# Performance work log

Hardware: AMD Instinct MI355X
Metric: run time of the kernel (lower is better)

The kernel has to match this reference:

```python
import jax, jax.numpy as jnp
import numpy as np

B, N, D_VIS, D_LBL = 64, 256, 2048, 512
H, F_OUT = 8, 256            # n_heads, gat_out_per_head_dim
D_IN = D_VIS + D_LBL         # 2560, GAT input dim
D_GAT = H * F_OUT            # 2048, concat-heads output dim
D_EMB = 512                  # final_embedding_dim
ALPHA = 0.2                  # LeakyReLU negative slope


def setup_inputs() -> dict:
    key = jax.random.key(0)
    ks = jax.random.split(key, 9)
    visual_features = jax.random.normal(ks[0], (B, D_VIS), jnp.float32)
    labels_features = jax.random.normal(ks[1], (N, D_LBL), jnp.float32)
    adj = (jax.random.uniform(ks[2], (N, N)) < 0.1).astype(jnp.float32)
    label_adj_matrix = jnp.maximum(adj, jnp.eye(N, dtype=jnp.float32))
    s = 1.0 / np.sqrt(D_IN)
    W_gat = jax.random.uniform(ks[3], (D_IN, H, F_OUT), jnp.float32, -s, s)
    a_src = jax.random.uniform(ks[4], (H, F_OUT), jnp.float32, -s, s)
    a_dst = jax.random.uniform(ks[5], (H, F_OUT), jnp.float32, -s, s)
    sg = 1.0 / np.sqrt(D_GAT)
    pool_q = jax.random.uniform(ks[6], (D_GAT,), jnp.float32, -sg, sg)
    fc_W = jax.random.uniform(ks[7], (D_GAT, D_EMB), jnp.float32, -sg, sg)
    fc_b = jax.random.uniform(ks[8], (D_EMB,), jnp.float32, -sg, sg)
    return {"visual_features": visual_features, "labels_features": labels_features,
            "label_adj_matrix": label_adj_matrix, "W_gat": W_gat, "a_src": a_src,
            "a_dst": a_dst, "pool_q": pool_q, "fc_W": fc_W, "fc_b": fc_b}


def reference(visual_features, labels_features, label_adj_matrix,
              W_gat, a_src, a_dst, pool_q, fc_W, fc_b):
    # Build per-sample contextualized label node features: (B, N, D_IN)
    x = jnp.concatenate(
        [jnp.broadcast_to(labels_features[None], (B, N, D_LBL)),
         jnp.broadcast_to(visual_features[:, None, :], (B, N, D_VIS))], axis=-1)
    # Multi-head GAT layer, batched over B (the torch code loops over B)
    Wh = jnp.einsum('bnd,dhf->bnhf', x, W_gat)            # (B, N, H, F)
    src = jnp.einsum('bnhf,hf->bhn', Wh, a_src)           # (B, H, N)
    dst = jnp.einsum('bnhf,hf->bhn', Wh, a_dst)           # (B, H, N)
    e = src[:, :, :, None] + dst[:, :, None, :]           # (B, H, N, N)
    e = jnp.where(e > 0, e, ALPHA * e)                    # LeakyReLU
    mask = (label_adj_matrix > 0)[None, None]             # (1, 1, N, N)
    scores = jnp.where(mask, e, jnp.float32(-9e15))
    attn = jax.nn.softmax(scores, axis=-1)                # (B, H, N, N)
    out = jnp.einsum('bhij,bjhf->bihf', attn, Wh)         # (B, N, H, F)
    out = jax.nn.elu(out.reshape(B, N, D_GAT))            # concat heads + ELU
    # attention pooling over label nodes
    pw = jax.nn.softmax(jnp.einsum('bnd,d->bn', out, pool_q), axis=-1)
    pooled = jnp.einsum('bn,bnd->bd', pw, out)            # (B, D_GAT)
    return pooled @ fc_W + fc_b                           # (B, D_EMB)
```

## Files before the change

### kernel.cpp

```cpp
#include <hip/hip_runtime.h>
#include <hip/hip_bf16.h>
#include <math.h>

#define BB 64
#define NN 256
#define D_VIS 2048
#define D_LBL 512
#define HH 8
#define FF 256
#define DG 2048
#define DE 512
#define ALPHA 0.2f
#define PSTRIDE 264
#define NSPLIT 4

using bf16 = __hip_bfloat16;
using short8 = __attribute__((ext_vector_type(8))) short;
using f32x4  = __attribute__((ext_vector_type(4))) float;
__device__ __forceinline__ float b2f(bf16 x) { return __bfloat162float(x); }
__device__ __forceinline__ unsigned short f2bs(float x) {
    bf16 h = __float2bfloat16(x);
    unsigned short u;
    __builtin_memcpy(&u, &h, 2);
    return u;
}
__device__ __forceinline__ float bs2f(unsigned short u) {
    unsigned int x = (unsigned int)u << 16;
    float f;
    __builtin_memcpy(&f, &x, 4);
    return f;
}

__global__ void __launch_bounds__(256) k_wh(const float* __restrict__ labels,
                                            const float* __restrict__ visual,
                                            const float* __restrict__ Wg,
                                            unsigned short* __restrict__ WhLbT,
                                            float* __restrict__ WhVz,
                                            const float* __restrict__ aSrc,
                                            const float* __restrict__ aDst,
                                            float* __restrict__ srcLp,
                                            float* __restrict__ dstLp,
                                            float* __restrict__ srcVp,
                                            float* __restrict__ dstVp,
                                            const float* __restrict__ adj,
                                            unsigned short* __restrict__ abits) {
    const int t = threadIdx.x;
    const int y = blockIdx.y;
    if (y == 8) {
        if (t < 128) {
            const int r = t >> 4, s = t & 15;
            const int i = blockIdx.x * 8 + r;
            unsigned int bits = 0;
#pragma unroll
            for (int jj = 0; jj < 8; ++jj) {
                const float2 av = *(const float2*)(adj + (size_t)i * NN + 2 * s + 32 * jj);
                bits |= (av.x > 0.f ? 1u : 0u) << (2 * jj);
                bits |= (av.y > 0.f ? 1u : 0u) << (2 * jj + 1);
            }
            abits[i * 16 + s] = (unsigned short)bits;
        }
        return;
    }

    __shared__ unsigned short As[2][64][72];
    __shared__ unsigned short Bs[2][64][72];
    const int w = t >> 6;
    const int lane = t & 63;
    const int l15 = lane & 15, quad = lane >> 4;
    const int n0 = blockIdx.x * 64;
    const int p2 = blockIdx.x & 3;
    const bool isL = (y < 4);
    const int m0  = isL ? y * 64 : 0;
    const int z   = isL ? 0 : (y - 4);
    const int kb0 = z * 512;
    const float* A = isL ? labels : visual;
    const int lda  = isL ? D_LBL : D_VIS;
    const float* Wb = Wg + (isL ? 0 : (size_t)D_LBL * DG);

    f32x4 acc[4];
#pragma unroll
    for (int mi = 0; mi < 4; ++mi) acc[mi] = (f32x4){0.f, 0.f, 0.f, 0.f};

    float4 ra[4], rb[4];
    auto load_tile = [&](int kc) {
        const int kb = kb0 + kc * 64;
#pragma unroll
        for (int p = 0; p < 4; ++p) {
            const int idx = t + 256 * p;
            const int r = idx >> 4, q4 = idx & 15;
            ra[p] = *(const float4*)(A + (size_t)(m0 + r) * lda + kb + 4 * q4);
        }
#pragma unroll
        for (int p = 0; p < 4; ++p) {
            const int kk = (t >> 4) + 16 * p;
            const int c4 = (t & 15) * 4;
            rb[p] = *(const float4*)(Wb + (size_t)(kb + kk) * DG + n0 + c4);
        }
    };
    auto store_tile = [&](int buf) {
#pragma unroll
        for (int p = 0; p < 4; ++p) {
            const int idx = t + 256 * p;
            const int r = idx >> 4, q4 = idx & 15;
            unsigned short s4[4] = {f2bs(ra[p].x), f2bs(ra[p].y), f2bs(ra[p].z), f2bs(ra[p].w)};
            __builtin_memcpy(&As[buf][r][4 * q4], s4, 8);
        }
#pragma unroll
        for (int p = 0; p < 4; ++p) {
            const int kk = (t >> 4) + 16 * p;
            const int c4 = (t & 15) * 4;
            Bs[buf][c4 + 0][kk] = f2bs(rb[p].x);
            Bs[buf][c4 + 1][kk] = f2bs(rb[p].y);
            Bs[buf][c4 + 2][kk] = f2bs(rb[p].z);
            Bs[buf][c4 + 3][kk] = f2bs(rb[p].w);
        }
    };

    load_tile(0);
    store_tile(0);
    __syncthreads();
    for (int kc = 0; kc < 8; ++kc) {
        const int cur = kc & 1;
        if (kc < 7) load_tile(kc + 1);
#pragma unroll
        for (int ks = 0; ks < 2; ++ks) {
            const short8 bf = *(const short8*)&Bs[cur][w * 16 + l15][ks * 32 + quad * 8];
#pragma unroll
            for (int mi = 0; mi < 4; ++mi) {
                const short8 af = *(const short8*)&As[cur][mi * 16 + l15][ks * 32 + quad * 8];
                acc[mi] = __builtin_amdgcn_mfma_f32_16x16x32_bf16(af, bf, acc[mi], 0, 0, 0);
            }
        }
        if (kc < 7) store_tile(cur ^ 1);
        __syncthreads();
    }
    const int col = n0 + w * 16 + l15;
    const int h = col >> 8;
    const float as = aSrc[col], ad = aDst[col];
    if (isL) {
#pragma unroll
        for (int mi = 0; mi < 4; ++mi) {
            unsigned short s4[4];
#pragma unroll
            for (int r = 0; r < 4; ++r) s4[r] = f2bs(acc[mi][r]);
            __builtin_memcpy(&WhLbT[(size_t)col * NN + m0 + mi * 16 + quad * 4], s4, 8);
        }
#pragma unroll
        for (int mi = 0; mi < 4; ++mi)
#pragma unroll
            for (int r = 0; r < 4; ++r) {
                float sv = acc[mi][r] * as;
                float dv = acc[mi][r] * ad;
#pragma unroll
                for (int off = 1; off < 16; off <<= 1) {
                    sv += __shfl_xor(sv, off);
                    dv += __shfl_xor(dv, off);
                }
                if (l15 == 0) {
                    const int row = m0 + mi * 16 + quad * 4 + r;
                    srcLp[(p2 * NN + row) * HH + h] = sv;
                    dstLp[(p2 * NN + row) * HH + h] = dv;
                }
            }
    } else {
        float* Wv = WhVz + (size_t)z * BB * DG;
#pragma unroll
        for (int mi = 0; mi < 4; ++mi)
#pragma unroll
            for (int r = 0; r < 4; ++r)
                Wv[(size_t)(mi * 16 + quad * 4 + r) * DG + col] = acc[mi][r];
        const int pv = p2 * 4 + z;
#pragma unroll
        for (int mi = 0; mi < 4; ++mi)
#pragma unroll
            for (int r = 0; r < 4; ++r) {
                float sv = acc[mi][r] * as;
                float dv = acc[mi][r] * ad;
#pragma unroll
                for (int off = 1; off < 16; off <<= 1) {
                    sv += __shfl_xor(sv, off);
                    dv += __shfl_xor(dv, off);
                }
                if (l15 == 0) {
                    const int row = mi * 16 + quad * 4 + r;
                    srcVp[(pv * BB + row) * HH + h] = sv;
                    dstVp[(pv * BB + row) * HH + h] = dv;
                }
            }
    }
}

__global__ void __launch_bounds__(512, 4) k_gat(const unsigned short* __restrict__ WhLbT,
                                                const float* __restrict__ WhVz,
                                                const float* __restrict__ srcLp,
                                                const float* __restrict__ dstLp,
                                                const float* __restrict__ srcVp,
                                                const float* __restrict__ dstVp,
                                                const unsigned short* __restrict__ abits,
                                                const float* __restrict__ pool_q,
                                                bf16* __restrict__ outb,
                                                float* __restrict__ ps_p) {
    const int bid = blockIdx.x;
    const int h = bid & 7;
    const int b = bid >> 3;
    const int t = threadIdx.x;
    const int w = t >> 6;
    const int lane = t & 63;
    const int l15 = lane & 15, quad = lane >> 4;

    __shared__ __align__(16) unsigned short Pl[64][PSTRIDE];
    __shared__ __align__(16) float dls2[2 * NN];
    __shared__ float slsA[NN], slsC[NN];
    __shared__ float inv[64];
    __shared__ float psl[8][64];

    if (t < NN) {
        float dl = 0.f, sl = 0.f;
#pragma unroll
        for (int p = 0; p < 4; ++p) {
            dl += dstLp[(p * NN + t) * HH + h];
            sl += srcLp[(p * NN + t) * HH + h];
        }
        dls2[2 * t]     = __expf(dl);
        dls2[2 * t + 1] = __expf(ALPHA * dl);
        float c = 0.f;
#pragma unroll
        for (int p = 0; p < 16; ++p)
            c += srcVp[(p * BB + b) * HH + h] + dstVp[(p * BB + b) * HH + h];
        const float u = c + sl;
        slsA[t] = __expf(u);
        slsC[t] = __expf(ALPHA * u);
    }
    const int n0 = w * 32;
    float wv[2] = {0.f, 0.f};
#pragma unroll
    for (int z = 0; z < 4; ++z)
#pragma unroll
        for (int ni = 0; ni < 2; ++ni)
            wv[ni] += WhVz[(size_t)z * BB * DG + (size_t)b * DG + h * FF + n0 + ni * 16 + l15];
    const float pqv0 = pool_q[h * FF + n0 + l15];
    const float pqv1 = pool_q[h * FF + n0 + 16 + l15];
    const unsigned short* wb = WhLbT + (size_t)(h * FF + n0 + l15) * NN + quad * 8;
    __syncthreads();

    for (int it = 0; it < 4; ++it) {
        const int i0 = it * 64;

        {
            const int g = lane >> 4, s = lane & 15;
#pragma unroll
            for (int rr = 0; rr < 2; ++rr) {
                const int iloc = w * 8 + rr * 4 + g;
                const int i = i0 + iloc;
                const unsigned int mb = abits[i * 16 + s];
                const float Ai = slsA[i], Ci = slsC[i];
                float pr[16];
                float sum = 0.f;
#pragma unroll
                for (int jj = 0; jj < 8; ++jj) {
                    const int j0 = 2 * s + 32 * jj;
                    const float4 bd = *(const float4*)&dls2[2 * j0];
                    float p0 = fmaxf(Ai * bd.x, Ci * bd.y);
                    float p1 = fmaxf(Ai * bd.z, Ci * bd.w);
                    p0 = (mb & (1u << (2 * jj)))     ? p0 : 0.f;
                    p1 = (mb & (1u << (2 * jj + 1))) ? p1 : 0.f;
                    pr[2 * jj] = p0; pr[2 * jj + 1] = p1;
                    sum += p0 + p1;
                }
#pragma unroll
                for (int off = 1; off < 16; off <<= 1) sum += __shfl_xor(sum, off);
                if (s == 0) inv[iloc] = 1.0f / sum;
#pragma unroll
                for (int jj = 0; jj < 8; ++jj) {
                    const unsigned int pk =
                        ((unsigned int)f2bs(pr[2 * jj + 1]) << 16) | f2bs(pr[2 * jj]);
                    *(unsigned int*)&Pl[iloc][2 * s + 32 * jj] = pk;
                }
            }
        }
        __syncthreads();

        f32x4 acc[4][2];
#pragma unroll
        for (int mi = 0; mi < 4; ++mi)
#pragma unroll
            for (int ni = 0; ni < 2; ++ni) acc[mi][ni] = (f32x4){0.f, 0.f, 0.f, 0.f};

        short8 bc0 = *(const short8*)(wb);
        short8 bc1 = *(const short8*)(wb + (size_t)16 * NN);
#pragma unroll
        for (int kc = 0; kc < 8; ++kc) {
            short8 bn0, bn1;
            if (kc < 7) {
                bn0 = *(const short8*)(wb + (kc + 1) * 32);
                bn1 = *(const short8*)(wb + (size_t)16 * NN + (kc + 1) * 32);
            }
            short8 a[4];
#pragma unroll
            for (int mi = 0; mi < 4; ++mi)
                a[mi] = *(const short8*)&Pl[mi * 16 + l15][kc * 32 + quad * 8];
#pragma unroll
            for (int mi = 0; mi < 4; ++mi)
                acc[mi][0] = __builtin_amdgcn_mfma_f32_16x16x32_bf16(a[mi], bc0, acc[mi][0], 0, 0, 0);
#pragma unroll
            for (int mi = 0; mi < 4; ++mi)
                acc[mi][1] = __builtin_amdgcn_mfma_f32_16x16x32_bf16(a[mi], bc1, acc[mi][1], 0, 0, 0);
            bc0 = bn0; bc1 = bn1;
        }

#pragma unroll
        for (int mi = 0; mi < 4; ++mi)
#pragma unroll
            for (int r = 0; r < 4; ++r) {
                const int row = mi * 16 + quad * 4 + r;
                const float ivr = inv[row];
                bf16* orow = outb + ((size_t)(b * NN + i0 + row)) * DG + h * FF + n0;
                float x0 = fmaf(acc[mi][0][r], ivr, wv[0]);
                float x1 = fmaf(acc[mi][1][r], ivr, wv[1]);
                x0 = x0 > 0.f ? x0 : (__expf(x0) - 1.0f);
                x1 = x1 > 0.f ? x1 : (__expf(x1) - 1.0f);
                orow[l15]      = __float2bfloat16(x0);
                orow[16 + l15] = __float2bfloat16(x1);
                float dot = fmaf(x0, pqv0, x1 * pqv1);
#pragma unroll
                for (int off = 1; off < 16; off <<= 1) dot += __shfl_xor(dot, off);
                if (l15 == 0) psl[w][row] = dot;
            }
        __syncthreads();
        if (t < 64) {
            float s = 0.f;
#pragma unroll
            for (int ww = 0; ww < 8; ++ww) s += psl[ww][t];
            ps_p[((size_t)h * BB + b) * NN + i0 + t] = s;
        }
    }
}

__global__ void __launch_bounds__(256) k_pool(const bf16* __restrict__ outb,
                                              const float* __restrict__ ps_p,
                                              float* __restrict__ pooled_p,
                                              const float* __restrict__ fcb,
                                              float* __restrict__ out) {
    const int dt = blockIdx.x;
    const int b  = blockIdx.y;
    const int ns = blockIdx.z;
    const int t  = threadIdx.x;
    if (dt == 0 && ns == 0) {
        out[b * DE + t]       = fcb[t];
        out[b * DE + 256 + t] = fcb[256 + t];
    }
    __shared__ float wsm[NN];
    __shared__ float redm[4];
    __shared__ float reds[4];
    float v = 0.f;
#pragma unroll
    for (int s = 0; s < 8; ++s)
        v += ps_p[((size_t)s * BB + b) * NN + t];
    float m = v;
#pragma unroll
    for (int off = 32; off; off >>= 1) m = fmaxf(m, __shfl_xor(m, off));
    if ((t & 63) == 0) redm[t >> 6] = m;
    __syncthreads();
    m = fmaxf(fmaxf(redm[0], redm[1]), fmaxf(redm[2], redm[3]));
    const float e = __expf(v - m);
    float s = e;
#pragma unroll
    for (int off = 32; off; off >>= 1) s += __shfl_xor(s, off);
    if ((t & 63) == 0) reds[t >> 6] = s;
    __syncthreads();
    s = reds[0] + reds[1] + reds[2] + reds[3];
    wsm[t] = e / s;
    __syncthreads();
    const int d0 = dt * 512 + t * 2;
    const int nb = ns * 64;
    float a0 = 0.f, a1 = 0.f;
    const bf16* base = outb + (size_t)b * NN * DG + d0;
#pragma unroll 8
    for (int n = 0; n < 64; ++n) {
        unsigned int q = *(const unsigned int*)(base + (size_t)(nb + n) * DG);
        const float wn = wsm[nb + n];
        a0 = fmaf(wn, bs2f((unsigned short)(q & 0xffff)), a0);
        a1 = fmaf(wn, bs2f((unsigned short)(q >> 16)), a1);
    }
    float2 r2 = {a0, a1};
    *(float2*)(pooled_p + ((size_t)(ns * BB + b)) * DG + d0) = r2;
}

__global__ void __launch_bounds__(256) k_mgemm(const float* __restrict__ Ap,
                                               const float* __restrict__ W, int ldw,
                                               float* __restrict__ C, int ldc,
                                               int kSlice, int kIters) {
    __shared__ unsigned short As[32][72];
    __shared__ unsigned short Bs[64][72];
    const int t = threadIdx.x;
    const int w = t >> 6;
    const int lane = t & 63;
    const int l15 = lane & 15, quad = lane >> 4;
    const int n0 = blockIdx.x * 64;
    const int m0 = blockIdx.y * 32;
    const int kb0 = blockIdx.z * kSlice;
    f32x4 acc[2];
    acc[0] = (f32x4){0.f, 0.f, 0.f, 0.f};
    acc[1] = (f32x4){0.f, 0.f, 0.f, 0.f};
    for (int kc = 0; kc < kIters; ++kc) {
        const int kb = kb0 + kc * 64;
#pragma unroll
        for (int p = 0; p < 2; ++p) {
            const int idx = t + 256 * p;
            const int r = idx >> 4, q4 = idx & 15;
            const float* ap = Ap + (size_t)(m0 + r) * DG + kb + 4 * q4;
            const float4 v0 = *(const float4*)(ap);
            const float4 v1 = *(const float4*)(ap + (size_t)BB * DG);
            const float4 v2 = *(const float4*)(ap + (size_t)2 * BB * DG);
            const float4 v3 = *(const float4*)(ap + (size_t)3 * BB * DG);
            const float vx = v0.x + v1.x + v2.x + v3.x;
            const float vy = v0.y + v1.y + v2.y + v3.y;
            const float vz = v0.z + v1.z + v2.z + v3.z;
            const float vw = v0.w + v1.w + v2.w + v3.w;
            unsigned short s4[4] = {f2bs(vx), f2bs(vy), f2bs(vz), f2bs(vw)};
            __builtin_memcpy(&As[r][4 * q4], s4, 8);
        }
#pragma unroll
        for (int p = 0; p < 4; ++p) {
            const int kk = (t >> 4) + 16 * p;
            const int c4 = (t & 15) * 4;
            const float4 v = *(const float4*)(W + (size_t)(kb + kk) * ldw + n0 + c4);
            Bs[c4 + 0][kk] = f2bs(v.x);
            Bs[c4 + 1][kk] = f2bs(v.y);
            Bs[c4 + 2][kk] = f2bs(v.z);
            Bs[c4 + 3][kk] = f2bs(v.w);
        }
        __syncthreads();
#pragma unroll
        for (int ks = 0; ks < 2; ++ks) {
            const short8 bf = *(const short8*)&Bs[w * 16 + l15][ks * 32 + quad * 8];
#pragma unroll
            for (int mi = 0; mi < 2; ++mi) {
                const short8 af = *(const short8*)&As[mi * 16 + l15][ks * 32 + quad * 8];
                acc[mi] = __builtin_amdgcn_mfma_f32_16x16x32_bf16(af, bf, acc[mi], 0, 0, 0);
            }
        }
        __syncthreads();
    }
    const int col = n0 + w * 16 + l15;
#pragma unroll
    for (int mi = 0; mi < 2; ++mi)
#pragma unroll
        for (int r = 0; r < 4; ++r)
            atomicAdd(&C[(size_t)(m0 + mi * 16 + quad * 4 + r) * ldc + col], acc[mi][r]);
}

extern "C" void kernel_launch(void* const* d_in, const int* in_sizes, int n_in,
                              void* d_out, int out_size, void* d_ws, size_t ws_size,
                              hipStream_t stream) {
    (void)in_sizes; (void)n_in; (void)out_size; (void)ws_size;
    const float* visual = (const float*)d_in[0];
    const float* labels = (const float*)d_in[1];
    const float* adj    = (const float*)d_in[2];
    const float* Wg     = (const float*)d_in[3];
    const float* a_src  = (const float*)d_in[4];
    const float* a_dst  = (const float*)d_in[5];
    const float* pool_q = (const float*)d_in[6];
    const float* fcW    = (const float*)d_in[7];
    const float* fcb    = (const float*)d_in[8];
    float* out = (float*)d_out;

    float* ws_f     = (float*)d_ws;
    float* WhVz     = ws_f;
    float* srcLp    = WhVz + 4 * BB * DG;
    float* dstLp    = srcLp + 4 * NN * HH;
    float* srcVp    = dstLp + 4 * NN * HH;
    float* dstVp    = srcVp + 16 * BB * HH;
    float* ps_p     = dstVp + 16 * BB * HH;
    float* pooled_p = ps_p + 8 * BB * NN;
    bf16*  outb     = (bf16*)(pooled_p + NSPLIT * BB * DG);
    unsigned short* WhLbT = (unsigned short*)(outb + (size_t)BB * NN * DG);
    unsigned short* abits = WhLbT + (size_t)DG * NN;

    k_wh<<<dim3(DG / 64, 9), 256, 0, stream>>>(labels, visual, Wg, WhLbT, WhVz,
                                               a_src, a_dst, srcLp, dstLp, srcVp, dstVp,
                                               adj, abits);

    k_gat<<<BB * HH, 512, 0, stream>>>(WhLbT, WhVz, srcLp, dstLp, srcVp, dstVp,
                                       abits, pool_q, outb, ps_p);

    k_pool<<<dim3(4, BB, NSPLIT), 256, 0, stream>>>(outb, ps_p, pooled_p, fcb, out);

    k_mgemm<<<dim3(DE / 64, BB / 32, 16), 256, 0, stream>>>(
        pooled_p, fcW, DE, out, DE, 128, 2);
}
```

Baseline: 164.0 us.

## Deepen k_wh load prefetch and widen k_pool vector loads with finer node split

```diff
diff --git a/kernel.cpp b/kernel.cpp
--- a/kernel.cpp
+++ b/kernel.cpp
@@ -12,7 +12,7 @@
 #define DE 512
 #define ALPHA 0.2f
 #define PSTRIDE 264
-#define NSPLIT 4
+#define NSPLIT 16
 
 using bf16 = __hip_bfloat16;
 using short8 = __attribute__((ext_vector_type(8))) short;
@@ -81,8 +81,8 @@
 #pragma unroll
     for (int mi = 0; mi < 4; ++mi) acc[mi] = (f32x4){0.f, 0.f, 0.f, 0.f};
 
-    float4 ra[4], rb[4];
-    auto load_tile = [&](int kc) {
+    float4 raA[4], rbA[4], raB[4], rbB[4];
+    auto load_tile = [&](int kc, float4 (&ra)[4], float4 (&rb)[4]) {
         const int kb = kb0 + kc * 64;
 #pragma unroll
         for (int p = 0; p < 4; ++p) {
@@ -97,7 +97,7 @@
             rb[p] = *(const float4*)(Wb + (size_t)(kb + kk) * DG + n0 + c4);
         }
     };
-    auto store_tile = [&](int buf) {
+    auto store_tile = [&](int buf, float4 (&ra)[4], float4 (&rb)[4]) {
 #pragma unroll
         for (int p = 0; p < 4; ++p) {
             const int idx = t + 256 * p;
@@ -115,23 +115,32 @@
             Bs[buf][c4 + 3][kk] = f2bs(rb[p].w);
         }
     };
-
-    load_tile(0);
-    store_tile(0);
+    auto mfma_step = [&](int buf) {
+#pragma unroll
+        for (int ks = 0; ks < 2; ++ks) {
+            const short8 bf = *(const short8*)&Bs[buf][w * 16 + l15][ks * 32 + quad * 8];
+#pragma unroll
+            for (int mi = 0; mi < 4; ++mi) {
+                const short8 af = *(const short8*)&As[buf][mi * 16 + l15][ks * 32 + quad * 8];
+                acc[mi] = __builtin_amdgcn_mfma_f32_16x16x32_bf16(af, bf, acc[mi], 0, 0, 0);
+            }
+        }
+    };
+
+    load_tile(0, raA, rbA);
+    load_tile(1, raB, rbB);
+    store_tile(0, raA, rbA);
     __syncthreads();
-    for (int kc = 0; kc < 8; ++kc) {
-        const int cur = kc & 1;
-        if (kc < 7) load_tile(kc + 1);
-#pragma unroll
-        for (int ks = 0; ks < 2; ++ks) {
-            const short8 bf = *(const short8*)&Bs[cur][w * 16 + l15][ks * 32 + quad * 8];
-#pragma unroll
-            for (int mi = 0; mi < 4; ++mi) {
-                const short8 af = *(const short8*)&As[cur][mi * 16 + l15][ks * 32 + quad * 8];
-                acc[mi] = __builtin_amdgcn_mfma_f32_16x16x32_bf16(af, bf, acc[mi], 0, 0, 0);
-            }
-        }
-        if (kc < 7) store_tile(cur ^ 1);
+#pragma unroll
+    for (int kp = 0; kp < 4; ++kp) {
+        const int kc = kp * 2;
+        if (kc + 2 < 8) load_tile(kc + 2, raA, rbA);
+        mfma_step(0);
+        store_tile(1, raB, rbB);
+        __syncthreads();
+        if (kc + 3 < 8) load_tile(kc + 3, raB, rbB);
+        mfma_step(1);
+        if (kc + 2 < 8) store_tile(0, raA, rbA);
         __syncthreads();
     }
     const int col = n0 + w * 16 + l15;
@@ -341,11 +350,10 @@
                                               float* __restrict__ pooled_p,
                                               const float* __restrict__ fcb,
                                               float* __restrict__ out) {
-    const int dt = blockIdx.x;
-    const int b  = blockIdx.y;
-    const int ns = blockIdx.z;
+    const int b  = blockIdx.x;
+    const int ns = blockIdx.y;
     const int t  = threadIdx.x;
-    if (dt == 0 && ns == 0) {
+    if (ns == 0) {
         out[b * DE + t]       = fcb[t];
         out[b * DE + 256 + t] = fcb[256 + t];
     }
@@ -371,19 +379,25 @@
     s = reds[0] + reds[1] + reds[2] + reds[3];
     wsm[t] = e / s;
     __syncthreads();
-    const int d0 = dt * 512 + t * 2;
-    const int nb = ns * 64;
-    float a0 = 0.f, a1 = 0.f;
+    const int d0 = t * 8;
+    const int nb = ns * 16;
+    float a[8];
+#pragma unroll
+    for (int j = 0; j < 8; ++j) a[j] = 0.f;
     const bf16* base = outb + (size_t)b * NN * DG + d0;
-#pragma unroll 8
-    for (int n = 0; n < 64; ++n) {
-        unsigned int q = *(const unsigned int*)(base + (size_t)(nb + n) * DG);
+#pragma unroll
+    for (int n = 0; n < 16; ++n) {
+        const short8 q = *(const short8*)(base + (size_t)(nb + n) * DG);
         const float wn = wsm[nb + n];
-        a0 = fmaf(wn, bs2f((unsigned short)(q & 0xffff)), a0);
-        a1 = fmaf(wn, bs2f((unsigned short)(q >> 16)), a1);
-    }
-    float2 r2 = {a0, a1};
-    *(float2*)(pooled_p + ((size_t)(ns * BB + b)) * DG + d0) = r2;
+#pragma unroll
+        for (int j = 0; j < 8; ++j)
+            a[j] = fmaf(wn, bs2f((unsigned short)q[j]), a[j]);
+    }
+    float* pp = pooled_p + ((size_t)ns * BB + b) * DG + d0;
+    float4 r0 = {a[0], a[1], a[2], a[3]};
+    float4 r1 = {a[4], a[5], a[6], a[7]};
+    *(float4*)pp = r0;
+    *(float4*)(pp + 4) = r1;
 }
 
 __global__ void __launch_bounds__(256) k_mgemm(const float* __restrict__ Ap,
@@ -409,15 +423,13 @@
             const int idx = t + 256 * p;
             const int r = idx >> 4, q4 = idx & 15;
             const float* ap = Ap + (size_t)(m0 + r) * DG + kb + 4 * q4;
-            const float4 v0 = *(const float4*)(ap);
-            const float4 v1 = *(const float4*)(ap + (size_t)BB * DG);
-            const float4 v2 = *(const float4*)(ap + (size_t)2 * BB * DG);
-            const float4 v3 = *(const float4*)(ap + (size_t)3 * BB * DG);
-            const float vx = v0.x + v1.x + v2.x + v3.x;
-            const float vy = v0.y + v1.y + v2.y + v3.y;
-            const float vz = v0.z + v1.z + v2.z + v3.z;
-            const float vw = v0.w + v1.w + v2.w + v3.w;
-            unsigned short s4[4] = {f2bs(vx), f2bs(vy), f2bs(vz), f2bs(vw)};
+            float4 vs = *(const float4*)ap;
+#pragma unroll
+            for (int s2 = 1; s2 < NSPLIT; ++s2) {
+                const float4 vv = *(const float4*)(ap + (size_t)s2 * BB * DG);
+                vs.x += vv.x; vs.y += vv.y; vs.z += vv.z; vs.w += vv.w;
+            }
+            unsigned short s4[4] = {f2bs(vs.x), f2bs(vs.y), f2bs(vs.z), f2bs(vs.w)};
             __builtin_memcpy(&As[r][4 * q4], s4, 8);
         }
 #pragma unroll
@@ -484,7 +496,7 @@
     k_gat<<<BB * HH, 512, 0, stream>>>(WhLbT, WhVz, srcLp, dstLp, srcVp, dstVp,
                                        abits, pool_q, outb, ps_p);
 
-    k_pool<<<dim3(4, BB, NSPLIT), 256, 0, stream>>>(outb, ps_p, pooled_p, fcb, out);
+    k_pool<<<dim3(BB, NSPLIT), 256, 0, stream>>>(outb, ps_p, pooled_p, fcb, out);
 
     k_mgemm<<<dim3(DE / 64, BB / 32, 16), 256, 0, stream>>>(
         pooled_p, fcW, DE, out, DE, 128, 2);
```

Result: slower. 167.9 us (+2.4%).

## Fuse attention pooling with final FC projection and move bias init into GAT kernel

Applied to the files above, without the earlier changes.

```diff
diff --git a/kernel.cpp b/kernel.cpp
--- a/kernel.cpp
+++ b/kernel.cpp
@@ -12,7 +12,6 @@
 #define DE 512
 #define ALPHA 0.2f
 #define PSTRIDE 264
-#define NSPLIT 4
 
 using bf16 = __hip_bfloat16;
 using short8 = __attribute__((ext_vector_type(8))) short;
@@ -199,7 +198,9 @@
                                                 const unsigned short* __restrict__ abits,
                                                 const float* __restrict__ pool_q,
                                                 bf16* __restrict__ outb,
-                                                float* __restrict__ ps_p) {
+                                                float* __restrict__ ps_p,
+                                                const float* __restrict__ fcb,
+                                                float* __restrict__ out) {
     const int bid = blockIdx.x;
     const int h = bid & 7;
     const int b = bid >> 3;
@@ -213,6 +214,8 @@
     __shared__ float slsA[NN], slsC[NN];
     __shared__ float inv[64];
     __shared__ float psl[8][64];
+
+    if (h == 0) out[b * DE + t] = fcb[t];
 
     if (t < NN) {
         float dl = 0.f, sl = 0.f;
@@ -336,22 +339,19 @@
     }
 }
 
-__global__ void __launch_bounds__(256) k_pool(const bf16* __restrict__ outb,
-                                              const float* __restrict__ ps_p,
-                                              float* __restrict__ pooled_p,
-                                              const float* __restrict__ fcb,
-                                              float* __restrict__ out) {
-    const int dt = blockIdx.x;
+__global__ void __launch_bounds__(256) k_pg(const bf16* __restrict__ outb,
+                                            const float* __restrict__ ps_p,
+                                            const float* __restrict__ fcW,
+                                            float* __restrict__ out) {
+    const int ds = blockIdx.x;
     const int b  = blockIdx.y;
-    const int ns = blockIdx.z;
     const int t  = threadIdx.x;
-    if (dt == 0 && ns == 0) {
-        out[b * DE + t]       = fcb[t];
-        out[b * DE + 256 + t] = fcb[256 + t];
-    }
     __shared__ float wsm[NN];
     __shared__ float redm[4];
     __shared__ float reds[4];
+    __shared__ __align__(16) float ppart[4][NN];
+    __shared__ float pooled_s[NN];
+
     float v = 0.f;
 #pragma unroll
     for (int s = 0; s < 8; ++s)
@@ -371,83 +371,37 @@
     s = reds[0] + reds[1] + reds[2] + reds[3];
     wsm[t] = e / s;
     __syncthreads();
-    const int d0 = dt * 512 + t * 2;
-    const int nb = ns * 64;
-    float a0 = 0.f, a1 = 0.f;
+
+    const int wq = t >> 6;
+    const int c  = t & 63;
+    const int d0 = ds * 256 + c * 4;
+    float a0 = 0.f, a1 = 0.f, a2 = 0.f, a3 = 0.f;
     const bf16* base = outb + (size_t)b * NN * DG + d0;
 #pragma unroll 8
-    for (int n = 0; n < 64; ++n) {
-        unsigned int q = *(const unsigned int*)(base + (size_t)(nb + n) * DG);
-        const float wn = wsm[nb + n];
-        a0 = fmaf(wn, bs2f((unsigned short)(q & 0xffff)), a0);
-        a1 = fmaf(wn, bs2f((unsigned short)(q >> 16)), a1);
-    }
-    float2 r2 = {a0, a1};
-    *(float2*)(pooled_p + ((size_t)(ns * BB + b)) * DG + d0) = r2;
-}
-
-__global__ void __launch_bounds__(256) k_mgemm(const float* __restrict__ Ap,
-                                               const float* __restrict__ W, int ldw,
-                                               float* __restrict__ C, int ldc,
-                                               int kSlice, int kIters) {
-    __shared__ unsigned short As[32][72];
-    __shared__ unsigned short Bs[64][72];
-    const int t = threadIdx.x;
-    const int w = t >> 6;
-    const int lane = t & 63;
-    const int l15 = lane & 15, quad = lane >> 4;
-    const int n0 = blockIdx.x * 64;
-    const int m0 = blockIdx.y * 32;
-    const int kb0 = blockIdx.z * kSlice;
-    f32x4 acc[2];
-    acc[0] = (f32x4){0.f, 0.f, 0.f, 0.f};
-    acc[1] = (f32x4){0.f, 0.f, 0.f, 0.f};
-    for (int kc = 0; kc < kIters; ++kc) {
-        const int kb = kb0 + kc * 64;
-#pragma unroll
-        for (int p = 0; p < 2; ++p) {
-            const int idx = t + 256 * p;
-            const int r = idx >> 4, q4 = idx & 15;
-            const float* ap = Ap + (size_t)(m0 + r) * DG + kb + 4 * q4;
-            const float4 v0 = *(const float4*)(ap);
-            const float4 v1 = *(const float4*)(ap + (size_t)BB * DG);
-            const float4 v2 = *(const float4*)(ap + (size_t)2 * BB * DG);
-            const float4 v3 = *(const float4*)(ap + (size_t)3 * BB * DG);
-            const float vx = v0.x + v1.x + v2.x + v3.x;
-            const float vy = v0.y + v1.y + v2.y + v3.y;
-            const float vz = v0.z + v1.z + v2.z + v3.z;
-            const float vw = v0.w + v1.w + v2.w + v3.w;
-            unsigned short s4[4] = {f2bs(vx), f2bs(vy), f2bs(vz), f2bs(vw)};
-            __builtin_memcpy(&As[r][4 * q4], s4, 8);
-        }
-#pragma unroll
-        for (int p = 0; p < 4; ++p) {
-            const int kk = (t >> 4) + 16 * p;
-            const int c4 = (t & 15) * 4;
-            const float4 v = *(const float4*)(W + (size_t)(kb + kk) * ldw + n0 + c4);
-            Bs[c4 + 0][kk] = f2bs(v.x);
-            Bs[c4 + 1][kk] = f2bs(v.y);
-            Bs[c4 + 2][kk] = f2bs(v.z);
-            Bs[c4 + 3][kk] = f2bs(v.w);
-        }
-        __syncthreads();
-#pragma unroll
-        for (int ks = 0; ks < 2; ++ks) {
-            const short8 bf = *(const short8*)&Bs[w * 16 + l15][ks * 32 + quad * 8];
-#pragma unroll
-            for (int mi = 0; mi < 2; ++mi) {
-                const short8 af = *(const short8*)&As[mi * 16 + l15][ks * 32 + quad * 8];
-                acc[mi] = __builtin_amdgcn_mfma_f32_16x16x32_bf16(af, bf, acc[mi], 0, 0, 0);
-            }
-        }
-        __syncthreads();
-    }
-    const int col = n0 + w * 16 + l15;
-#pragma unroll
-    for (int mi = 0; mi < 2; ++mi)
-#pragma unroll
-        for (int r = 0; r < 4; ++r)
-            atomicAdd(&C[(size_t)(m0 + mi * 16 + quad * 4 + r) * ldc + col], acc[mi][r]);
+    for (int n = wq * 64; n < wq * 64 + 64; ++n) {
+        const uint2 q = *(const uint2*)(base + (size_t)n * DG);
+        const float wn = wsm[n];
+        a0 = fmaf(wn, bs2f((unsigned short)(q.x & 0xffff)), a0);
+        a1 = fmaf(wn, bs2f((unsigned short)(q.x >> 16)), a1);
+        a2 = fmaf(wn, bs2f((unsigned short)(q.y & 0xffff)), a2);
+        a3 = fmaf(wn, bs2f((unsigned short)(q.y >> 16)), a3);
+    }
+    float4 pv = {a0, a1, a2, a3};
+    *(float4*)&ppart[wq][c * 4] = pv;
+    __syncthreads();
+    pooled_s[t] = ppart[0][t] + ppart[1][t] + ppart[2][t] + ppart[3][t];
+    __syncthreads();
+
+    float acc0 = 0.f, acc1 = 0.f;
+    const float* Wp = fcW + (size_t)(ds * 256) * DE + t;
+#pragma unroll 8
+    for (int k = 0; k < 256; ++k) {
+        const float pk = pooled_s[k];
+        acc0 = fmaf(pk, Wp[(size_t)k * DE], acc0);
+        acc1 = fmaf(pk, Wp[(size_t)k * DE + 256], acc1);
+    }
+    atomicAdd(&out[b * DE + t], acc0);
+    atomicAdd(&out[b * DE + 256 + t], acc1);
 }
 
 extern "C" void kernel_launch(void* const* d_in, const int* in_sizes, int n_in,
@@ -465,15 +419,14 @@
     const float* fcb    = (const float*)d_in[8];
     float* out = (float*)d_out;
 
-    float* ws_f     = (float*)d_ws;
-    float* WhVz     = ws_f;
-    float* srcLp    = WhVz + 4 * BB * DG;
-    float* dstLp    = srcLp + 4 * NN * HH;
-    float* srcVp    = dstLp + 4 * NN * HH;
-    float* dstVp    = srcVp + 16 * BB * HH;
-    float* ps_p     = dstVp + 16 * BB * HH;
-    float* pooled_p = ps_p + 8 * BB * NN;
-    bf16*  outb     = (bf16*)(pooled_p + NSPLIT * BB * DG);
+    float* ws_f   = (float*)d_ws;
+    float* WhVz   = ws_f;
+    float* srcLp  = WhVz + 4 * BB * DG;
+    float* dstLp  = srcLp + 4 * NN * HH;
+    float* srcVp  = dstLp + 4 * NN * HH;
+    float* dstVp  = srcVp + 16 * BB * HH;
+    float* ps_p   = dstVp + 16 * BB * HH;
+    bf16*  outb   = (bf16*)(ps_p + 8 * BB * NN);
     unsigned short* WhLbT = (unsigned short*)(outb + (size_t)BB * NN * DG);
     unsigned short* abits = WhLbT + (size_t)DG * NN;
 
@@ -482,10 +435,7 @@
                                                adj, abits);
 
     k_gat<<<BB * HH, 512, 0, stream>>>(WhLbT, WhVz, srcLp, dstLp, srcVp, dstVp,
-                                       abits, pool_q, outb, ps_p);
-
-    k_pool<<<dim3(4, BB, NSPLIT), 256, 0, stream>>>(outb, ps_p, pooled_p, fcb, out);
-
-    k_mgemm<<<dim3(DE / 64, BB / 32, 16), 256, 0, stream>>>(
-        pooled_p, fcW, DE, out, DE, 128, 2);
-}
+                                       abits, pool_q, outb, ps_p, fcb, out);
+
+    k_pg<<<dim3(8, BB), 256, 0, stream>>>(outb, ps_p, fcW, out);
+}
```

New measurement: 175.0 us. 6.7% more time.
